# Kernel optimization log

Measured on AMD Instinct MI355X. Metric: run time of the kernel, lower is better.

The kernel has to match this reference:

```python
import jax, jax.numpy as jnp
import numpy as np

WS = 8      # window size
NH = 8      # num heads
DIM = 256   # channels
HD = DIM // NH  # head dim = 32


def _rel_idx():
    ws = WS
    coords = np.stack(np.meshgrid(np.arange(ws), np.arange(ws), indexing='ij'))
    flat = coords.reshape(2, -1)
    rel = (flat[:, :, None] - flat[:, None, :]).transpose(1, 2, 0).copy()
    rel[..., 0] += ws - 1
    rel[..., 1] += ws - 1
    rel[..., 0] *= 2 * ws - 1
    return jnp.asarray(rel.sum(-1))  # [ws*ws, ws*ws]

REL_IDX = _rel_idx()


def _conv(x, w, b=None, pad=0, groups=1):
    out = jax.lax.conv_general_dilated(x, w, (1, 1), [(pad, pad), (pad, pad)],
                                       feature_group_count=groups,
                                       dimension_numbers=('NCHW', 'OIHW', 'NCHW'))
    if b is not None:
        out = out + b[None, :, None, None]
    return out


def _pw(w, x):  # 1x1 conv, no bias
    return jnp.einsum('oc,bchw->bohw', w, x)


def _adaptive_avg_pool(x, s):  # torch AdaptiveAvgPool2d((s,s)) semantics
    B, C, H, W = x.shape
    rows = []
    for i in range(s):
        h0, h1 = (i * H) // s, -((-(i + 1) * H) // s)
        cols = []
        for j in range(s):
            w0, w1 = (j * W) // s, -((-(j + 1) * W) // s)
            cols.append(x[:, :, h0:h1, w0:w1].mean(axis=(2, 3)))
        rows.append(jnp.stack(cols, axis=-1))
    return jnp.stack(rows, axis=-2)  # [B,C,s,s]


def _lowpass(v_img):  # LowPassModule: 4-way channel split, pyramid pool + bilinear up, relu
    B, C, H, W = v_img.shape
    ch = C // 4
    outs = []
    for i, s in enumerate((1, 2, 3, 6)):
        p = _adaptive_avg_pool(v_img[:, i * ch:(i + 1) * ch], s)
        outs.append(jax.image.resize(p, (B, ch, H, W), method='bilinear'))
    return jax.nn.relu(jnp.concatenate(outs, axis=1))


def _avgpool(x, kh, kw, ph, pw):  # AvgPool2d, stride 1, count_include_pad=True
    s = jax.lax.reduce_window(x, 0.0, jax.lax.add, (1, 1, kh, kw), (1, 1, 1, 1),
                              ((0, 0), (0, 0), (ph, ph), (pw, pw)))
    return s / (kh * kw)


def _forward(x, qkv_w, ld1_w, ld2_w, camax_w1, camax_b1, camax_w2, camax_b2,
             caavg_w1, caavg_b1, caavg_w2, caavg_b2, sa_w, sa_b,
             f3_w, f3_b, f5_w, f5_b, f7_w, f7_b, rel_table, dw_w, bn_g, bn_b, pw_w):
    B, C, H, W = x.shape
    ws, h = WS, NH
    d = C // h
    scale = d ** -0.5
    hh, ww = H // ws, W // ws
    # ---- local branch: 1x1 expand -> CBAM -> 1x1 reduce ----
    loc = _pw(ld1_w, x)  # [B,2C,H,W]
    mx = loc.max(axis=(2, 3))
    av = loc.mean(axis=(2, 3))
    wmax = jax.nn.sigmoid(jax.nn.relu(mx @ camax_w1.T + camax_b1) @ camax_w2.T + camax_b2)
    wavg = jax.nn.sigmoid(jax.nn.relu(av @ caavg_w1.T + caavg_b1) @ caavg_w2.T + caavg_b2)
    loc = jax.nn.sigmoid(wmax + wavg)[:, :, None, None] * loc
    cat = jnp.stack([loc.max(axis=1), loc.mean(axis=1)], axis=1)  # [B,2,H,W]
    loc = jax.nn.sigmoid(_conv(cat, sa_w, sa_b, pad=3)) * loc
    loc = _pw(ld2_w, loc)  # [B,C,H,W]
    # ---- windowed qkv (H,W divisible by ws -> reflect pad is a no-op) ----
    qkv = _pw(qkv_w, x)  # [B,3C,H,W]
    t = qkv.reshape(B, 3, h, d, hh, ws, ww, ws)
    t = t.transpose(1, 0, 4, 6, 2, 5, 7, 3).reshape(3, B * hh * ww, h, ws * ws, d)
    q, k = t[0], t[1]
    # df path uses channel decomposition (qkv c h), NOT (qkv h d)
    t2 = qkv.reshape(B, 3, d, h, H * W).transpose(1, 0, 3, 4, 2)  # [3,B,h,N,d]
    df_q, df_v = t2[0], t2[2]
    dots = jnp.einsum('whld,whmd->whlm', q, k) * scale
    bias = rel_table[REL_IDX.reshape(-1)].reshape(ws * ws, ws * ws, h).transpose(2, 0, 1)
    attn = jax.nn.softmax(dots + bias[None], axis=-1)
    # ---- dynamic hi/lo-pass filter ----
    v_img = df_v.transpose(0, 1, 3, 2).reshape(B, h * d, H, W)
    LP = _lowpass(v_img).reshape(B, h, d, H * W).transpose(0, 1, 3, 2)  # [B,h,N,d]
    o1, o2 = 2 * d, 5 * d  # channel splits [64,96,96]
    HP = jnp.concatenate([
        _conv(v_img[:, :o1], f3_w, f3_b, pad=1, groups=o1),
        _conv(v_img[:, o1:o2], f5_w, f5_b, pad=2, groups=3 * d),
        _conv(v_img[:, o2:], f7_w, f7_b, pad=3, groups=3 * d)], axis=1)
    HP = HP.reshape(B, h, d, H * W).transpose(0, 1, 3, 2)
    df = df_q * HP + LP  # [B,h,N,d]
    dfw = df.reshape(B, h, hh, ws, ww, ws, d).transpose(0, 2, 4, 1, 3, 5, 6)
    dfw = dfw.reshape(B * hh * ww, h, ws * ws, d)
    av2 = jnp.einsum('whlm,whmd->whld', attn, dfw)
    img = av2.reshape(B, hh, ww, h, ws, ws, d).transpose(0, 3, 6, 1, 4, 2, 5).reshape(B, C, H, W)
    # ---- directional average pooling + local fuse ----
    px = jnp.pad(img, ((0, 0), (0, 0), (0, 1), (0, 0)), mode='reflect')
    py = jnp.pad(img, ((0, 0), (0, 0), (0, 0), (0, 1)), mode='reflect')
    out = _avgpool(px, ws, 1, ws // 2 - 1, 0) + _avgpool(py, 1, ws, 0, ws // 2 - 1)
    out = out + loc
    out = jnp.pad(out, ((0, 0), (0, 0), (0, 1), (0, 1)), mode='reflect')
    # ---- proj: depthwise k=8 -> BN (eval, running stats 0/1) -> 1x1 ----
    out = _conv(out, dw_w, pad=3, groups=C)
    out = out * (bn_g / jnp.sqrt(1.0 + 1e-5))[None, :, None, None] + bn_b[None, :, None, None]
    out = _pw(pw_w, out)
    return out[:, :, :H, :W]


def setup_inputs() -> dict:
    key = jax.random.key(0)
    ks = jax.random.split(key, 26)
    B, C, H, W = 4, DIM, 128, 128
    d = HD
    f = lambda k, shape, s=0.05: jax.random.normal(k, shape, dtype=jnp.float32) * s
    return {
        'x': jax.random.normal(ks[0], (B, C, H, W), dtype=jnp.float32),
        'qkv_w': f(ks[1], (3 * C, C)),
        'ld1_w': f(ks[2], (2 * C, C)),
        'ld2_w': f(ks[3], (C, 2 * C)),
        'camax_w1': f(ks[4], (C, 2 * C)), 'camax_b1': f(ks[5], (C,)),
        'camax_w2': f(ks[6], (2 * C, C)), 'camax_b2': f(ks[7], (2 * C,)),
        'caavg_w1': f(ks[8], (C, 2 * C)), 'caavg_b1': f(ks[9], (C,)),
        'caavg_w2': f(ks[10], (2 * C, C)), 'caavg_b2': f(ks[11], (2 * C,)),
        'sa_w': f(ks[12], (1, 2, 7, 7)), 'sa_b': f(ks[13], (1,)),
        'f3_w': f(ks[14], (2 * d, 1, 3, 3)), 'f3_b': f(ks[15], (2 * d,)),
        'f5_w': f(ks[16], (3 * d, 1, 5, 5)), 'f5_b': f(ks[17], (3 * d,)),
        'f7_w': f(ks[18], (3 * d, 1, 7, 7)), 'f7_b': f(ks[19], (3 * d,)),
        'rel_table': f(ks[20], ((2 * WS - 1) * (2 * WS - 1), NH), 0.02),
        'dw_w': f(ks[21], (C, 1, WS, WS)),
        'bn_g': 1.0 + f(ks[22], (C,)), 'bn_b': f(ks[23], (C,)),
        'pw_w': f(ks[24], (C, C)),
    }


def reference(x, qkv_w, ld1_w, ld2_w, camax_w1, camax_b1, camax_w2, camax_b2,
              caavg_w1, caavg_b1, caavg_w2, caavg_b2, sa_w, sa_b,
              f3_w, f3_b, f5_w, f5_b, f7_w, f7_b, rel_table, dw_w, bn_g, bn_b, pw_w):
    return _forward(x, qkv_w, ld1_w, ld2_w, camax_w1, camax_b1, camax_w2, camax_b2,
                    caavg_w1, caavg_b1, caavg_w2, caavg_b2, sa_w, sa_b,
                    f3_w, f3_b, f5_w, f5_b, f7_w, f7_b, rel_table, dw_w, bn_g, bn_b, pw_w)
```

## Files before the change

### kernel.cpp

```cpp
#include <hip/hip_runtime.h>
#include <hip/hip_bf16.h>
#include <math.h>

#define B_ 4
#define H_ 128
#define W_ 128
#define N_ 16384

using bf16 = __hip_bfloat16;
typedef short short8 __attribute__((ext_vector_type(8)));
typedef short s16x4 __attribute__((ext_vector_type(4)));
typedef float f32x4 __attribute__((ext_vector_type(4)));

__device__ __forceinline__ float toF(float v) { return v; }
__device__ __forceinline__ float toF(bf16 v) { return __bfloat162float(v); }
__device__ __forceinline__ void storeF(float* p, float v) { *p = v; }
__device__ __forceinline__ void storeF(bf16* p, float v) { *p = __float2bfloat16(v); }

__device__ __forceinline__ unsigned short f2bf(float f) {
  unsigned u = __builtin_bit_cast(unsigned, f);
  unsigned r = (u + 0x7FFFu + ((u >> 16) & 1u)) >> 16;
  return (unsigned short)r;
}
__device__ __forceinline__ short rawbf(float v) { return (short)f2bf(v); }
__device__ __forceinline__ short rawbf(bf16 v) { return __builtin_bit_cast(short, v); }
__device__ __forceinline__ float bfs2f(short s) {
  return __builtin_bit_cast(float, ((unsigned)(unsigned short)s) << 16);
}

__device__ __forceinline__ short8 ld8(const bf16* p) { return *(const short8*)p; }

__device__ __forceinline__ void st8f(float* dst, short8 v) {
  float4 a, b2;
  a.x = bfs2f(v[0]); a.y = bfs2f(v[1]); a.z = bfs2f(v[2]); a.w = bfs2f(v[3]);
  b2.x = bfs2f(v[4]); b2.y = bfs2f(v[5]); b2.z = bfs2f(v[6]); b2.w = bfs2f(v[7]);
  *(float4*)dst = a;
  *(float4*)(dst + 4) = b2;
}

template <typename TX, typename TY>
__global__ __launch_bounds__(256) void gemm_mfma(
    const bf16* __restrict__ Wb, const TX* __restrict__ X, TY* __restrict__ Y, int IC) {
  __shared__ short smA[8192];
  __shared__ short smB[8192];
  int tid = threadIdx.x;
  int lane = tid & 63, w = tid >> 6;
  int wm = w >> 1, wn = w & 1;
  int n0 = blockIdx.x * 128, oc0 = blockIdx.y * 128, b = blockIdx.z;
  const TX* Xb = X + (size_t)b * IC * N_;
  TY* Yb = Y + (size_t)b * (gridDim.y * 128) * N_;
  f32x4 acc[4][4] = {};
  int nB = tid & 127;
  int gB0 = tid >> 7;

  for (int k0 = 0; k0 < IC; k0 += 64) {
    short8 areg[4], breg[4];
#pragma unroll
    for (int i = 0; i < 4; i++) {
      int q = i * 256 + tid;
      int rowA = q >> 3, gA = q & 7;
      areg[i] = ld8(Wb + (size_t)(oc0 + rowA) * IC + k0 + gA * 8);
      int gB = i * 2 + gB0;
      const TX* src = Xb + (size_t)(k0 + gB * 8) * N_ + n0 + nB;
      short8 v;
#pragma unroll
      for (int j = 0; j < 8; j++) v[j] = rawbf(src[(size_t)j * N_]);
      breg[i] = v;
    }
    __syncthreads();
#pragma unroll
    for (int i = 0; i < 4; i++) {
      int q = i * 256 + tid;
      int rowA = q >> 3, gA = q & 7;
      *(short8*)&smA[rowA * 64 + ((gA ^ (rowA & 7)) * 8)] = areg[i];
      int gB = i * 2 + gB0;
      *(short8*)&smB[nB * 64 + ((gB ^ (nB & 7)) * 8)] = breg[i];
    }
    __syncthreads();
#pragma unroll
    for (int ks = 0; ks < 2; ks++) {
      int gk = ks * 4 + (lane >> 4);
      short8 af[4], bfr[4];
#pragma unroll
      for (int mf = 0; mf < 4; mf++) {
        int row = wm * 64 + mf * 16 + (lane & 15);
        af[mf] = *(const short8*)&smA[row * 64 + ((gk ^ (row & 7)) * 8)];
      }
#pragma unroll
      for (int nf = 0; nf < 4; nf++) {
        int nr = wn * 64 + nf * 16 + (lane & 15);
        bfr[nf] = *(const short8*)&smB[nr * 64 + ((gk ^ (nr & 7)) * 8)];
      }
#pragma unroll
      for (int nf = 0; nf < 4; nf++)
#pragma unroll
        for (int mf = 0; mf < 4; mf++)
          acc[mf][nf] = __builtin_amdgcn_mfma_f32_16x16x32_bf16(af[mf], bfr[nf], acc[mf][nf], 0, 0, 0);
    }
    __syncthreads();
  }
#pragma unroll
  for (int mf = 0; mf < 4; mf++)
#pragma unroll
    for (int nf = 0; nf < 4; nf++) {
      int ocr = oc0 + wm * 64 + mf * 16 + ((lane >> 4) << 2);
      int nc = n0 + wn * 64 + nf * 16 + (lane & 15);
#pragma unroll
      for (int j = 0; j < 4; j++)
        storeF(&Yb[(size_t)(ocr + j) * N_ + nc], acc[mf][nf][j]);
    }
}

__global__ __launch_bounds__(256) void gemm_mfmaT(
    const bf16* __restrict__ Wb, const bf16* __restrict__ XT, bf16* __restrict__ Y, int IC) {
  __shared__ short smA[8192];
  __shared__ short smB[8192];
  int tid = threadIdx.x;
  int lane = tid & 63, w = tid >> 6;
  int wm = w >> 1, wn = w & 1;
  int n0 = blockIdx.x * 128, oc0 = blockIdx.y * 128, b = blockIdx.z;
  const bf16* Xb = XT + (size_t)b * N_ * IC;
  bf16* Yb = Y + (size_t)b * (gridDim.y * 128) * N_;
  f32x4 acc[4][4] = {};

  for (int k0 = 0; k0 < IC; k0 += 64) {
    short8 areg[4], breg[4];
#pragma unroll
    for (int i = 0; i < 4; i++) {
      int q = i * 256 + tid;
      int rowA = q >> 3, gA = q & 7;
      areg[i] = ld8(Wb + (size_t)(oc0 + rowA) * IC + k0 + gA * 8);
      breg[i] = ld8(Xb + (size_t)(n0 + rowA) * IC + k0 + gA * 8);
    }
    __syncthreads();
#pragma unroll
    for (int i = 0; i < 4; i++) {
      int q = i * 256 + tid;
      int rowA = q >> 3, gA = q & 7;
      int so = (gA ^ (rowA & 7)) * 8;
      *(short8*)&smA[rowA * 64 + so] = areg[i];
      *(short8*)&smB[rowA * 64 + so] = breg[i];
    }
    __syncthreads();
#pragma unroll
    for (int ks = 0; ks < 2; ks++) {
      int gk = ks * 4 + (lane >> 4);
      short8 af[4], bfr[4];
#pragma unroll
      for (int mf = 0; mf < 4; mf++) {
        int row = wm * 64 + mf * 16 + (lane & 15);
        af[mf] = *(const short8*)&smA[row * 64 + ((gk ^ (row & 7)) * 8)];
      }
#pragma unroll
      for (int nf = 0; nf < 4; nf++) {
        int nr = wn * 64 + nf * 16 + (lane & 15);
        bfr[nf] = *(const short8*)&smB[nr * 64 + ((gk ^ (nr & 7)) * 8)];
      }
#pragma unroll
      for (int nf = 0; nf < 4; nf++)
#pragma unroll
        for (int mf = 0; mf < 4; mf++)
          acc[mf][nf] = __builtin_amdgcn_mfma_f32_16x16x32_bf16(af[mf], bfr[nf], acc[mf][nf], 0, 0, 0);
    }
    __syncthreads();
  }
#pragma unroll
  for (int mf = 0; mf < 4; mf++)
#pragma unroll
    for (int nf = 0; nf < 4; nf++) {
      int ocr = oc0 + wm * 64 + mf * 16 + ((lane >> 4) << 2);
      int nc = n0 + wn * 64 + nf * 16 + (lane & 15);
#pragma unroll
      for (int j = 0; j < 4; j++)
        storeF(&Yb[(size_t)(ocr + j) * N_ + nc], acc[mf][nf][j]);
    }
}

__global__ __launch_bounds__(256) void gemm_qkvT(
    const bf16* __restrict__ Wb, const bf16* __restrict__ XT, bf16* __restrict__ Y, int IC) {
  __shared__ short smA[8192];
  __shared__ short smB[8192];
  int tid = threadIdx.x;
  int lane = tid & 63, w = tid >> 6;
  int wm = w >> 1, wn = w & 1;
  int n0 = blockIdx.x * 128, oc0 = blockIdx.y * 128, b = blockIdx.z;
  const bf16* Xb = XT + (size_t)b * N_ * IC;
  bf16* Yb = Y + (size_t)b * 768 * N_;
  f32x4 acc[4][4] = {};

  for (int k0 = 0; k0 < IC; k0 += 64) {
    short8 areg[4], breg[4];
#pragma unroll
    for (int i = 0; i < 4; i++) {
      int q = i * 256 + tid;
      int rowA = q >> 3, gA = q & 7;
      areg[i] = ld8(Wb + (size_t)(oc0 + rowA) * IC + k0 + gA * 8);
      breg[i] = ld8(Xb + (size_t)(n0 + rowA) * IC + k0 + gA * 8);
    }
    __syncthreads();
#pragma unroll
    for (int i = 0; i < 4; i++) {
      int q = i * 256 + tid;
      int rowA = q >> 3, gA = q & 7;
      int so = (gA ^ (rowA & 7)) * 8;
      *(short8*)&smA[rowA * 64 + so] = areg[i];
      *(short8*)&smB[rowA * 64 + so] = breg[i];
    }
    __syncthreads();
#pragma unroll
    for (int ks = 0; ks < 2; ks++) {
      int gk = ks * 4 + (lane >> 4);
      short8 af[4], bfr[4];
#pragma unroll
      for (int mf = 0; mf < 4; mf++) {
        int row = wm * 64 + mf * 16 + (lane & 15);
        af[mf] = *(const short8*)&smA[row * 64 + ((gk ^ (row & 7)) * 8)];
      }
#pragma unroll
      for (int nf = 0; nf < 4; nf++) {
        int nr = wn * 64 + nf * 16 + (lane & 15);
        bfr[nf] = *(const short8*)&smB[nr * 64 + ((gk ^ (nr & 7)) * 8)];
      }
#pragma unroll
      for (int nf = 0; nf < 4; nf++)
#pragma unroll
        for (int mf = 0; mf < 4; mf++)
          acc[mf][nf] = __builtin_amdgcn_mfma_f32_16x16x32_bf16(af[mf], bfr[nf], acc[mf][nf], 0, 0, 0);
    }
    __syncthreads();
  }
  if (oc0 >= 256 && oc0 < 512) {
    bf16* kT = Yb + (size_t)256 * N_;
#pragma unroll
    for (int mf = 0; mf < 4; mf++)
#pragma unroll
      for (int nf = 0; nf < 4; nf++) {
        int ocr = oc0 + wm * 64 + mf * 16 + ((lane >> 4) << 2);
        int nc = n0 + wn * 64 + nf * 16 + (lane & 15);
        int koff = ocr - 256;
        int head = koff >> 5, dc = koff & 31;
        s16x4 ov;
#pragma unroll
        for (int j = 0; j < 4; j++) ov[j] = rawbf(acc[mf][nf][j]);
        *(s16x4*)&kT[((size_t)head * N_ + nc) * 32 + dc] = ov;
      }
  } else {
#pragma unroll
    for (int mf = 0; mf < 4; mf++)
#pragma unroll
      for (int nf = 0; nf < 4; nf++) {
        int ocr = oc0 + wm * 64 + mf * 16 + ((lane >> 4) << 2);
        int nc = n0 + wn * 64 + nf * 16 + (lane & 15);
#pragma unroll
        for (int j = 0; j < 4; j++)
          storeF(&Yb[(size_t)(ocr + j) * N_ + nc], acc[mf][nf][j]);
      }
  }
}

template <typename TX>
__global__ __launch_bounds__(256) void gemm_qkv(
    const bf16* __restrict__ Wb, const TX* __restrict__ X, bf16* __restrict__ Y, int IC) {
  __shared__ short smA[8192];
  __shared__ short smB[8192];
  int tid = threadIdx.x;
  int lane = tid & 63, w = tid >> 6;
  int wm = w >> 1, wn = w & 1;
  int n0 = blockIdx.x * 128, oc0 = blockIdx.y * 128, b = blockIdx.z;
  const TX* Xb = X + (size_t)b * IC * N_;
  bf16* Yb = Y + (size_t)b * 768 * N_;
  f32x4 acc[4][4] = {};
  int nB = tid & 127;
  int gB0 = tid >> 7;

  for (int k0 = 0; k0 < IC; k0 += 64) {
    short8 areg[4], breg[4];
#pragma unroll
    for (int i = 0; i < 4; i++) {
      int q = i * 256 + tid;
      int rowA = q >> 3, gA = q & 7;
      areg[i] = ld8(Wb + (size_t)(oc0 + rowA) * IC + k0 + gA * 8);
      int gB = i * 2 + gB0;
      const TX* src = Xb + (size_t)(k0 + gB * 8) * N_ + n0 + nB;
      short8 v;
#pragma unroll
      for (int j = 0; j < 8; j++) v[j] = rawbf(src[(size_t)j * N_]);
      breg[i] = v;
    }
    __syncthreads();
#pragma unroll
    for (int i = 0; i < 4; i++) {
      int q = i * 256 + tid;
      int rowA = q >> 3, gA = q & 7;
      *(short8*)&smA[rowA * 64 + ((gA ^ (rowA & 7)) * 8)] = areg[i];
      int gB = i * 2 + gB0;
      *(short8*)&smB[nB * 64 + ((gB ^ (nB & 7)) * 8)] = breg[i];
    }
    __syncthreads();
#pragma unroll
    for (int ks = 0; ks < 2; ks++) {
      int gk = ks * 4 + (lane >> 4);
      short8 af[4], bfr[4];
#pragma unroll
      for (int mf = 0; mf < 4; mf++) {
        int row = wm * 64 + mf * 16 + (lane & 15);
        af[mf] = *(const short8*)&smA[row * 64 + ((gk ^ (row & 7)) * 8)];
      }
#pragma unroll
      for (int nf = 0; nf < 4; nf++) {
        int nr = wn * 64 + nf * 16 + (lane & 15);
        bfr[nf] = *(const short8*)&smB[nr * 64 + ((gk ^ (nr & 7)) * 8)];
      }
#pragma unroll
      for (int nf = 0; nf < 4; nf++)
#pragma unroll
        for (int mf = 0; mf < 4; mf++)
          acc[mf][nf] = __builtin_amdgcn_mfma_f32_16x16x32_bf16(af[mf], bfr[nf], acc[mf][nf], 0, 0, 0);
    }
    __syncthreads();
  }
  if (oc0 >= 256 && oc0 < 512) {
    bf16* kT = Yb + (size_t)256 * N_;
#pragma unroll
    for (int mf = 0; mf < 4; mf++)
#pragma unroll
      for (int nf = 0; nf < 4; nf++) {
        int ocr = oc0 + wm * 64 + mf * 16 + ((lane >> 4) << 2);
        int nc = n0 + wn * 64 + nf * 16 + (lane & 15);
        int koff = ocr - 256;
        int head = koff >> 5, dc = koff & 31;
        s16x4 ov;
#pragma unroll
        for (int j = 0; j < 4; j++) ov[j] = rawbf(acc[mf][nf][j]);
        *(s16x4*)&kT[((size_t)head * N_ + nc) * 32 + dc] = ov;
      }
  } else {
#pragma unroll
    for (int mf = 0; mf < 4; mf++)
#pragma unroll
      for (int nf = 0; nf < 4; nf++) {
        int ocr = oc0 + wm * 64 + mf * 16 + ((lane >> 4) << 2);
        int nc = n0 + wn * 64 + nf * 16 + (lane & 15);
#pragma unroll
        for (int j = 0; j < 4; j++)
          storeF(&Yb[(size_t)(ocr + j) * N_ + nc], acc[mf][nf][j]);
      }
  }
}

__global__ __launch_bounds__(256) void gemm_mfma_sc(
    const bf16* __restrict__ Wb, const bf16* __restrict__ X, bf16* __restrict__ Y, int IC,
    const float* __restrict__ svec, const float* __restrict__ samap) {
  __shared__ short smA[8192];
  __shared__ short smB[8192];
  int tid = threadIdx.x;
  int lane = tid & 63, w = tid >> 6;
  int wm = w >> 1, wn = w & 1;
  int n0 = blockIdx.x * 128, oc0 = blockIdx.y * 128, b = blockIdx.z;
  const bf16* Xb = X + (size_t)b * IC * N_;
  bf16* Yb = Y + (size_t)b * (gridDim.y * 128) * N_;
  f32x4 acc[4][4] = {};
  int nB = tid & 127;
  int gB0 = tid >> 7;
  const float* sv = svec + b * 512;
  float sm = samap[b * N_ + n0 + nB];

  for (int k0 = 0; k0 < IC; k0 += 64) {
    short8 areg[4], breg[4];
#pragma unroll
    for (int i = 0; i < 4; i++) {
      int q = i * 256 + tid;
      int rowA = q >> 3, gA = q & 7;
      areg[i] = ld8(Wb + (size_t)(oc0 + rowA) * IC + k0 + gA * 8);
      int gB = i * 2 + gB0;
      int c0 = k0 + gB * 8;
      const bf16* src = Xb + (size_t)c0 * N_ + n0 + nB;
      short8 v;
#pragma unroll
      for (int j = 0; j < 8; j++)
        v[j] = rawbf(bfs2f(rawbf(src[(size_t)j * N_])) * sv[c0 + j] * sm);
      breg[i] = v;
    }
    __syncthreads();
#pragma unroll
    for (int i = 0; i < 4; i++) {
      int q = i * 256 + tid;
      int rowA = q >> 3, gA = q & 7;
      *(short8*)&smA[rowA * 64 + ((gA ^ (rowA & 7)) * 8)] = areg[i];
      int gB = i * 2 + gB0;
      *(short8*)&smB[nB * 64 + ((gB ^ (nB & 7)) * 8)] = breg[i];
    }
    __syncthreads();
#pragma unroll
    for (int ks = 0; ks < 2; ks++) {
      int gk = ks * 4 + (lane >> 4);
      short8 af[4], bfr[4];
#pragma unroll
      for (int mf = 0; mf < 4; mf++) {
        int row = wm * 64 + mf * 16 + (lane & 15);
        af[mf] = *(const short8*)&smA[row * 64 + ((gk ^ (row & 7)) * 8)];
      }
#pragma unroll
      for (int nf = 0; nf < 4; nf++) {
        int nr = wn * 64 + nf * 16 + (lane & 15);
        bfr[nf] = *(const short8*)&smB[nr * 64 + ((gk ^ (nr & 7)) * 8)];
      }
#pragma unroll
      for (int nf = 0; nf < 4; nf++)
#pragma unroll
        for (int mf = 0; mf < 4; mf++)
          acc[mf][nf] = __builtin_amdgcn_mfma_f32_16x16x32_bf16(af[mf], bfr[nf], acc[mf][nf], 0, 0, 0);
    }
    __syncthreads();
  }
#pragma unroll
  for (int mf = 0; mf < 4; mf++)
#pragma unroll
    for (int nf = 0; nf < 4; nf++) {
      int ocr = oc0 + wm * 64 + mf * 16 + ((lane >> 4) << 2);
      int nc = n0 + wn * 64 + nf * 16 + (lane & 15);
#pragma unroll
      for (int j = 0; j < 4; j++)
        storeF(&Yb[(size_t)(ocr + j) * N_ + nc], acc[mf][nf][j]);
    }
}

__global__ __launch_bounds__(256) void k_cvt(const float* __restrict__ s,
                                             bf16* __restrict__ d, int n) {
  int i = blockIdx.x * 256 + threadIdx.x;
  if (i < n) d[i] = __float2bfloat16(s[i]);
}

__global__ __launch_bounds__(256) void k_cvtT(const float* __restrict__ x,
                                              bf16* __restrict__ xT) {
  int ct = blockIdx.x, nt = blockIdx.y, b = blockIdx.z;
  int c0 = ct * 64, n0 = nt * 128;
  __shared__ float t[64][129];
  int tid = threadIdx.x;
  const float* xb_ = x + ((size_t)b * 256 + c0) * N_ + n0;
#pragma unroll
  for (int i = 0; i < 8; i++) {
    int q = i * 256 + tid;
    int r = q >> 5, col4 = q & 31;
    float4 v = *(const float4*)&xb_[(size_t)r * N_ + col4 * 4];
    t[r][col4 * 4 + 0] = v.x; t[r][col4 * 4 + 1] = v.y;
    t[r][col4 * 4 + 2] = v.z; t[r][col4 * 4 + 3] = v.w;
  }
  __syncthreads();
  bf16* dst = xT + ((size_t)b * N_ + n0) * 256 + c0;
#pragma unroll
  for (int i = 0; i < 4; i++) {
    int q = i * 256 + tid;
    int nl = q >> 3, oct = q & 7;
    short8 v;
#pragma unroll
    for (int j = 0; j < 8; j++) v[j] = rawbf(t[oct * 8 + j][nl]);
    *(short8*)&dst[(size_t)nl * 256 + oct * 8] = v;
  }
}

template <int S>
__device__ __forceinline__ void lp_body(const bf16* __restrict__ src,
                                        float* __restrict__ poolout,
                                        float (*part)[6], int tid) {
  int row = tid >> 1, xh = (tid & 1) << 6;
  float partial[6] = {0.f, 0.f, 0.f, 0.f, 0.f, 0.f};
  const bf16* rp = src + row * W_ + xh;
#pragma unroll
  for (int o = 0; o < 8; o++) {
    short8 v = ld8(rp + o * 8);
#pragma unroll
    for (int e = 0; e < 8; e++) {
      float f = bfs2f(v[e]);
      int x = xh + o * 8 + e;
#pragma unroll
      for (int j = 0; j < S; j++) {
        int w0 = (j * W_) / S;
        int w1 = ((j + 1) * W_ + S - 1) / S;
        if (x >= w0 && x < w1) partial[j] += f;
      }
    }
  }
#pragma unroll
  for (int j = 0; j < S; j++) part[tid][j] = partial[j];
  __syncthreads();
  if (tid < S * S) {
    int i = tid / S, j = tid % S;
    int h0 = (i * H_) / S, h1 = ((i + 1) * H_ + S - 1) / S;
    int w0 = (j * W_) / S, w1 = ((j + 1) * W_ + S - 1) / S;
    float sum = 0.f;
    for (int r2 = h0; r2 < h1; r2++) sum += part[r2 * 2][j] + part[r2 * 2 + 1][j];
    poolout[tid] = sum / (float)((h1 - h0) * (w1 - w0));
  }
}

__global__ __launch_bounds__(256) void k_lp_pool(const bf16* __restrict__ qkv,
                                                 float* __restrict__ pools) {
  int cc = blockIdx.x, b = blockIdx.y;
  __shared__ float part[256][6];
  int vch = 512 + (cc & 31) * 8 + (cc >> 5);
  const bf16* src = qkv + ((size_t)b * 768 + vch) * N_;
  float* po = pools + ((size_t)b * 256 + cc) * 36;
  int tid = threadIdx.x;
  int g = cc >> 6;
  if (g == 0)      lp_body<1>(src, po, part, tid);
  else if (g == 1) lp_body<2>(src, po, part, tid);
  else if (g == 2) lp_body<3>(src, po, part, tid);
  else             lp_body<6>(src, po, part, tid);
}

template <int KSZ>
__device__ __forceinline__ void hp_conv4(const float (*patch)[136], const float* wsm,
                                         int rs4, int cg4, float acc[4][4]) {
  constexpr int ROFF = 3 - KSZ / 2;
  constexpr int COFF = 4 - KSZ / 2;
#pragma unroll
  for (int pr = ROFF; pr < ROFF + KSZ + 3; pr++) {
    float val[12];
    const float* row = &patch[rs4 + pr][cg4];
    *(float4*)&val[0] = *(const float4*)&row[0];
    *(float4*)&val[4] = *(const float4*)&row[4];
    *(float4*)&val[8] = *(const float4*)&row[8];
#pragma unroll
    for (int j = 0; j < 4; j++) {
      int u = pr - ROFF - j;
      if (u >= 0 && u < KSZ) {
#pragma unroll
        for (int v = 0; v < KSZ; v++) {
          float wv = wsm[u * KSZ + v];
#pragma unroll
          for (int c = 0; c < 4; c++) acc[j][c] += val[c + v + COFF] * wv;
        }
      }
    }
  }
}

__global__ __launch_bounds__(256) void k_dffuse(const bf16* __restrict__ qkv,
    const float* __restrict__ pools,
    const float* __restrict__ f3w, const float* __restrict__ f3b,
    const float* __restrict__ f5w, const float* __restrict__ f5b,
    const float* __restrict__ f7w, const float* __restrict__ f7b,
    bf16* __restrict__ df) {
  int b = blockIdx.z, cc = blockIdx.y, ty0 = blockIdx.x * 32;
  __shared__ float patch[38][136];
  __shared__ float wsm[49];
  int tid = threadIdx.x;
  int vch = 512 + (cc & 31) * 8 + (cc >> 5);
  const bf16* src = qkv + ((size_t)b * 768 + vch) * N_;
  int ksz; const float* wp; float bias;
  if (cc < 64)       { ksz = 3; wp = f3w + cc * 9;          bias = f3b[cc]; }
  else if (cc < 160) { ksz = 5; wp = f5w + (cc - 64) * 25;  bias = f5b[cc - 64]; }
  else               { ksz = 7; wp = f7w + (cc - 160) * 49; bias = f7b[cc - 160]; }
  if (tid < ksz * ksz) wsm[tid] = wp[tid];
  float4 z4 = make_float4(0.f, 0.f, 0.f, 0.f);
  for (int i4 = tid; i4 < 1292; i4 += 256) ((float4*)patch)[i4] = z4;
  __syncthreads();
  for (int slot = tid; slot < 38 * 16; slot += 256) {
    int py = slot >> 4, seg = slot & 15;
    int gy = ty0 - 3 + py;
    if (gy >= 0 && gy < H_)
      st8f(&patch[py][4 + seg * 8], ld8(&src[gy * W_ + seg * 8]));
  }
  __syncthreads();
  int rs4 = (tid >> 5) * 4, cg4 = (tid & 31) * 4;
  float acc[4][4] = {{bias, bias, bias, bias}, {bias, bias, bias, bias},
                     {bias, bias, bias, bias}, {bias, bias, bias, bias}};
  if (cc < 64)       hp_conv4<3>(patch, wsm, rs4, cg4, acc);
  else if (cc < 160) hp_conv4<5>(patch, wsm, rs4, cg4, acc);
  else               hp_conv4<7>(patch, wsm, rs4, cg4, acc);
  const int S[4] = {1, 2, 3, 6};
  int s = S[cc >> 6];
  const float* pl = pools + ((size_t)b * 256 + cc) * 36;
  int qch = (cc & 31) * 8 + (cc >> 5);
  const bf16* qsrc = qkv + ((size_t)b * 768 + qch) * N_;
#pragma unroll
  for (int j = 0; j < 4; j++) {
    int y = ty0 + rs4 + j;
    float fy = (y + 0.5f) * s * (1.0f / 128.f) - 0.5f;
    int i0r = (int)floorf(fy); float tyf = fy - i0r;
    int i1 = min(max(i0r + 1, 0), s - 1);
    int i0 = min(max(i0r, 0), s - 1);
    s16x4 qv = *(const s16x4*)&qsrc[y * W_ + cg4];
    s16x4 ov;
#pragma unroll
    for (int c = 0; c < 4; c++) {
      int x = cg4 + c;
      float fx = (x + 0.5f) * s * (1.0f / 128.f) - 0.5f;
      int j0r = (int)floorf(fx); float txf = fx - j0r;
      int j1 = min(max(j0r + 1, 0), s - 1);
      int j0 = min(max(j0r, 0), s - 1);
      float v00 = pl[i0 * s + j0], v01 = pl[i0 * s + j1];
      float v10 = pl[i1 * s + j0], v11 = pl[i1 * s + j1];
      float lp = (1.f - tyf) * ((1.f - txf) * v00 + txf * v01) +
                 tyf * ((1.f - txf) * v10 + txf * v11);
      lp = fmaxf(lp, 0.f);
      ov[c] = rawbf(bfs2f(qv[c]) * acc[j][c] + lp);
    }
    *(s16x4*)&df[((size_t)b * 256 + cc) * N_ + y * W_ + cg4] = ov;
  }
}

__global__ __launch_bounds__(256) void k_attn(const bf16* __restrict__ qkv,
    bf16* __restrict__ df, const float* __restrict__ rel) {
  int b = blockIdx.z, head = blockIdx.y, wg = blockIdx.x;
  int wh = wg >> 2, wc4 = wg & 3;
  __shared__ short P[4][4096];
  __shared__ float biasLds[4][228];
  int tid = threadIdx.x, lane = tid & 63, w = tid >> 6;
  int wc = wc4 * 4 + w;
  short* Pw = P[w];
  float* bw = biasLds[w];
  int lr = lane & 15, lo = lane >> 4;
  int nwin = (wh * 8) * W_ + wc * 8;
  for (int i = lane; i < 225; i += 64) bw[i] = rel[i * 8 + head];
  const bf16* qb = qkv + ((size_t)b * 768 + head * 32 + lo * 8) * N_;
  const bf16* kT = qkv + ((size_t)b * 768 + 256) * N_ + (size_t)head * N_ * 32;
  short8 af[4], bf4[4];
#pragma unroll
  for (int mf = 0; mf < 4; mf++) {
    int l = mf * 16 + lr;
    int n = nwin + (l >> 3) * W_ + (l & 7);
#pragma unroll
    for (int j = 0; j < 8; j++) af[mf][j] = rawbf(qb[(size_t)j * N_ + n]);
    bf4[mf] = ld8(&kT[(size_t)n * 32 + lo * 8]);
  }
  const bf16* dbase = df + ((size_t)b * 256 + head * 32) * N_;
  short8 db[2][2];
#pragma unroll
  for (int ks = 0; ks < 2; ks++)
#pragma unroll
    for (int nf = 0; nf < 2; nf++) {
      int dc = nf * 16 + lr;
      int r = ks * 4 + lo;
      db[ks][nf] = ld8(dbase + (size_t)dc * N_ + nwin + r * W_);
    }
  f32x4 acc[4][4] = {};
#pragma unroll
  for (int nf = 0; nf < 4; nf++)
#pragma unroll
    for (int mf = 0; mf < 4; mf++)
      acc[mf][nf] = __builtin_amdgcn_mfma_f32_16x16x32_bf16(af[mf], bf4[nf], acc[mf][nf], 0, 0, 0);
  const float scale = 0.17677669529663687f;
#pragma unroll
  for (int mf = 0; mf < 4; mf++)
#pragma unroll
    for (int j = 0; j < 4; j++) {
      int lrow = mf * 16 + lo * 4 + j;
      int r1 = lrow >> 3, c1 = lrow & 7;
#pragma unroll
      for (int nf = 0; nf < 4; nf++) {
        int m = nf * 16 + lr;
        acc[mf][nf][j] = acc[mf][nf][j] * scale +
                         bw[(r1 - (m >> 3) + 7) * 15 + (c1 - (m & 7) + 7)];
      }
      float mx = fmaxf(fmaxf(acc[mf][0][j], acc[mf][1][j]),
                       fmaxf(acc[mf][2][j], acc[mf][3][j]));
      mx = fmaxf(mx, __shfl_xor(mx, 1));
      mx = fmaxf(mx, __shfl_xor(mx, 2));
      mx = fmaxf(mx, __shfl_xor(mx, 4));
      mx = fmaxf(mx, __shfl_xor(mx, 8));
      float s = 0.f;
#pragma unroll
      for (int nf = 0; nf < 4; nf++) {
        acc[mf][nf][j] = __expf(acc[mf][nf][j] - mx);
        s += acc[mf][nf][j];
      }
      s += __shfl_xor(s, 1); s += __shfl_xor(s, 2);
      s += __shfl_xor(s, 4); s += __shfl_xor(s, 8);
      float inv = 1.0f / s;
#pragma unroll
      for (int nf = 0; nf < 4; nf++) {
        int m = nf * 16 + lr;
        Pw[lrow * 64 + (((m >> 3) ^ (lrow & 7)) * 8) + (m & 7)] = rawbf(acc[mf][nf][j] * inv);
      }
    }
  __syncthreads();
  f32x4 acc2[4][2] = {};
#pragma unroll
  for (int ks = 0; ks < 2; ks++) {
    short8 pa[4];
#pragma unroll
    for (int mf = 0; mf < 4; mf++) {
      int row = mf * 16 + lr;
      pa[mf] = *(const short8*)&Pw[row * 64 + (((ks * 4 + lo) ^ (row & 7)) * 8)];
    }
#pragma unroll
    for (int nf = 0; nf < 2; nf++)
#pragma unroll
      for (int mf = 0; mf < 4; mf++)
        acc2[mf][nf] = __builtin_amdgcn_mfma_f32_16x16x32_bf16(pa[mf], db[ks][nf], acc2[mf][nf], 0, 0, 0);
  }
#pragma unroll
  for (int mf = 0; mf < 4; mf++)
#pragma unroll
    for (int nf = 0; nf < 2; nf++) {
      int ll = mf * 16 + lo * 4;
      int dc = nf * 16 + lr;
      s16x4 ov;
#pragma unroll
      for (int j = 0; j < 4; j++) ov[j] = rawbf(acc2[mf][nf][j]);
      int n = nwin + (ll >> 3) * W_ + (ll & 7);
      *(s16x4*)&df[((size_t)b * 256 + head * 32 + dc) * N_ + n] = ov;
    }
}

__global__ __launch_bounds__(256) void k_chstats(const bf16* __restrict__ loc,
    float* __restrict__ mx, float* __restrict__ av) {
  int c = blockIdx.x, b = blockIdx.y;
  const bf16* p = loc + ((size_t)b * 512 + c) * N_;
  int tid = threadIdx.x;
  float m = -1e30f, s = 0.f;
  for (int i = tid * 8; i < N_; i += 2048) {
    short8 v = *(const short8*)&p[i];
#pragma unroll
    for (int j = 0; j < 8; j++) { float f = bfs2f(v[j]); m = fmaxf(m, f); s += f; }
  }
  __shared__ float rm[256], rs[256];
  rm[tid] = m; rs[tid] = s;
  __syncthreads();
  for (int off = 128; off > 0; off >>= 1) {
    if (tid < off) {
      rm[tid] = fmaxf(rm[tid], rm[tid + off]);
      rs[tid] += rs[tid + off];
    }
    __syncthreads();
  }
  if (tid == 0) { mx[b * 512 + c] = rm[0]; av[b * 512 + c] = rs[0] / (float)N_; }
}

__global__ __launch_bounds__(256) void k_mlp1(const float* __restrict__ mx,
    const float* __restrict__ av,
    const float* __restrict__ w1m, const float* __restrict__ b1m,
    const float* __restrict__ w1a, const float* __restrict__ b1a,
    float* __restrict__ hidden) {
  int path = blockIdx.z, b = blockIdx.y, j0 = blockIdx.x * 64;
  const float* stats = (path ? av : mx) + b * 512;
  const float* w1 = path ? w1a : w1m;
  const float* b1 = path ? b1a : b1m;
  int tid = threadIdx.x, lane = tid & 63, wv = tid >> 6;
#pragma unroll
  for (int jj = 0; jj < 16; jj++) {
    int j = j0 + wv * 16 + jj;
    float a = 0.f;
#pragma unroll
    for (int t = 0; t < 8; t++) {
      int i = lane + t * 64;
      a += stats[i] * w1[j * 512 + i];
    }
#pragma unroll
    for (int off = 32; off > 0; off >>= 1) a += __shfl_xor(a, off);
    if (lane == 0) hidden[(path * 4 + b) * 256 + j] = fmaxf(a + b1[j], 0.f);
  }
}

__global__ __launch_bounds__(256) void k_mlp2(const float* __restrict__ hidden,
    const float* __restrict__ w2m, const float* __restrict__ b2m,
    const float* __restrict__ w2a, const float* __restrict__ b2a,
    float* __restrict__ svec) {
  int b = blockIdx.y, o0 = blockIdx.x * 64;
  const float* hm = hidden + b * 256;
  const float* ha = hidden + (4 + b) * 256;
  int tid = threadIdx.x, lane = tid & 63, wv = tid >> 6;
#pragma unroll
  for (int oo = 0; oo < 16; oo++) {
    int o = o0 + wv * 16 + oo;
    float sm = 0.f, sa = 0.f;
#pragma unroll
    for (int t = 0; t < 4; t++) {
      int jj = lane + t * 64;
      sm += hm[jj] * w2m[o * 256 + jj];
      sa += ha[jj] * w2a[o * 256 + jj];
    }
#pragma unroll
    for (int off = 32; off > 0; off >>= 1) {
      sm += __shfl_xor(sm, off);
      sa += __shfl_xor(sa, off);
    }
    if (lane == 0) {
      float wm = 1.f / (1.f + __expf(-(sm + b2m[o])));
      float wa = 1.f / (1.f + __expf(-(sa + b2a[o])));
      svec[b * 512 + o] = 1.f / (1.f + __expf(-(wm + wa)));
    }
  }
}

__global__ __launch_bounds__(256) void k_cat(const bf16* __restrict__ loc,
    const float* __restrict__ svec, float* __restrict__ catmax, float* __restrict__ catmean) {
  int b = blockIdx.y;
  int n2 = (blockIdx.x * 256 + threadIdx.x) * 2;
  const bf16* lb = loc + (size_t)b * 512 * N_;
  const float* sv = svec + b * 512;
  float m0 = -1e30f, m1 = -1e30f, s0 = 0.f, s1 = 0.f;
#pragma unroll 4
  for (int c = 0; c < 512; c++) {
    unsigned u = *(const unsigned*)&lb[(size_t)c * N_ + n2];
    float sc = sv[c];
    float f0 = __builtin_bit_cast(float, u << 16) * sc;
    float f1 = __builtin_bit_cast(float, u & 0xffff0000u) * sc;
    m0 = fmaxf(m0, f0); s0 += f0;
    m1 = fmaxf(m1, f1); s1 += f1;
  }
  catmax[b * N_ + n2] = m0;     catmax[b * N_ + n2 + 1] = m1;
  catmean[b * N_ + n2] = s0 * (1.f / 512.f);
  catmean[b * N_ + n2 + 1] = s1 * (1.f / 512.f);
}

__global__ __launch_bounds__(256) void k_sa(const float* __restrict__ catmax,
    const float* __restrict__ catmean, const float* __restrict__ saw,
    const float* __restrict__ sab, float* __restrict__ samap) {
  int b = blockIdx.y;
  int n = blockIdx.x * 256 + threadIdx.x;
  int y = n >> 7, x = n & 127;
  float acc = sab[0];
  for (int u = 0; u < 7; u++) {
    int yy = y + u - 3;
    if (yy < 0 || yy >= H_) continue;
    for (int v = 0; v < 7; v++) {
      int xx = x + v - 3;
      if (xx < 0 || xx >= W_) continue;
      int nn = b * N_ + yy * W_ + xx;
      acc += catmax[nn] * saw[u * 7 + v] + catmean[nn] * saw[49 + u * 7 + v];
    }
  }
  samap[b * N_ + n] = 1.f / (1.f + __expf(-acc));
}

__global__ __launch_bounds__(256) void k_out1(const bf16* __restrict__ img,
    const bf16* __restrict__ locout, bf16* __restrict__ out1) {
  int b = blockIdx.z, c = blockIdx.y, ty0 = blockIdx.x * 32;
  __shared__ float patch[39][136];
  int tid = threadIdx.x;
  const bf16* p = img + ((size_t)b * 256 + c) * N_;
  float4 z4 = make_float4(0.f, 0.f, 0.f, 0.f);
  for (int i4 = tid; i4 < 1326; i4 += 256) ((float4*)patch)[i4] = z4;
  __syncthreads();
  for (int slot = tid; slot < 39 * 16; slot += 256) {
    int py = slot >> 4, seg = slot & 15;
    int gy = ty0 - 3 + py;
    if (gy >= 0 && gy <= 128) {
      int yy = (gy == 128) ? 126 : gy;
      st8f(&patch[py][4 + seg * 8], ld8(&p[yy * W_ + seg * 8]));
    }
  }
  if (tid < 39) {
    int gy = ty0 - 3 + tid;
    if (gy >= 0 && gy <= 128) {
      int yy = (gy == 128) ? 126 : gy;
      patch[tid][132] = toF(p[yy * W_ + 126]);
    }
  }
  __syncthreads();
  int rs4 = (tid >> 5) * 4, cg4 = (tid & 31) * 4;
  float accv[4][4] = {};
  float acch[4][4] = {};
#pragma unroll
  for (int pr = 0; pr < 11; pr++) {
    float val[12];
    const float* row = &patch[rs4 + pr][cg4];
    *(float4*)&val[0] = *(const float4*)&row[0];
    *(float4*)&val[4] = *(const float4*)&row[4];
    *(float4*)&val[8] = *(const float4*)&row[8];
#pragma unroll
    for (int j = 0; j < 4; j++) {
      int u = pr - j;
      if (u >= 0 && u < 8) {
#pragma unroll
        for (int cc2 = 0; cc2 < 4; cc2++) accv[j][cc2] += val[cc2 + 4];
        if (u == 3) {
#pragma unroll
          for (int off = 1; off <= 8; off++)
#pragma unroll
            for (int cc2 = 0; cc2 < 4; cc2++) acch[j][cc2] += val[cc2 + off];
        }
      }
    }
  }
#pragma unroll
  for (int j = 0; j < 4; j++) {
    int y = ty0 + rs4 + j;
    size_t o = ((size_t)b * 256 + c) * N_ + y * W_ + cg4;
    s16x4 lo = *(const s16x4*)&locout[o];
    s16x4 ov;
#pragma unroll
    for (int cc2 = 0; cc2 < 4; cc2++)
      ov[cc2] = rawbf(0.125f * (accv[j][cc2] + acch[j][cc2]) + bfs2f(lo[cc2]));
    *(s16x4*)&out1[o] = ov;
  }
}

__global__ __launch_bounds__(256) void k_dw(const bf16* __restrict__ out1,
    const float* __restrict__ dww, const float* __restrict__ bng,
    const float* __restrict__ bnb, bf16* __restrict__ dwo) {
  int b = blockIdx.z, c = blockIdx.y, ty0 = blockIdx.x * 32;
  __shared__ float patch[39][136];
  __shared__ float wsm[64];
  int tid = threadIdx.x;
  const bf16* p = out1 + ((size_t)b * 256 + c) * N_;
  if (tid < 64) wsm[tid] = dww[c * 64 + tid];
  float4 z4 = make_float4(0.f, 0.f, 0.f, 0.f);
  for (int i4 = tid; i4 < 1326; i4 += 256) ((float4*)patch)[i4] = z4;
  __syncthreads();
  for (int slot = tid; slot < 39 * 16; slot += 256) {
    int py = slot >> 4, seg = slot & 15;
    int gy = ty0 - 3 + py;
    if (gy >= 0 && gy <= 128) {
      int yy = (gy == 128) ? 126 : gy;
      st8f(&patch[py][4 + seg * 8], ld8(&p[yy * W_ + seg * 8]));
    }
  }
  if (tid < 39) {
    int gy = ty0 - 3 + tid;
    if (gy >= 0 && gy <= 128) {
      int yy = (gy == 128) ? 126 : gy;
      patch[tid][132] = toF(p[yy * W_ + 126]);
    }
  }
  __syncthreads();
  int rs4 = (tid >> 5) * 4, cg4 = (tid & 31) * 4;
  float acc[4][4] = {};
#pragma unroll
  for (int pr = 0; pr < 11; pr++) {
    float val[12];
    const float* row = &patch[rs4 + pr][cg4];
    *(float4*)&val[0] = *(const float4*)&row[0];
    *(float4*)&val[4] = *(const float4*)&row[4];
    *(float4*)&val[8] = *(const float4*)&row[8];
#pragma unroll
    for (int j = 0; j < 4; j++) {
      int u = pr - j;
      if (u >= 0 && u < 8) {
#pragma unroll
        for (int v = 0; v < 8; v++) {
          float wv = wsm[u * 8 + v];
#pragma unroll
          for (int cc2 = 0; cc2 < 4; cc2++) acc[j][cc2] += val[cc2 + v + 1] * wv;
        }
      }
    }
  }
  float g = bng[c] * rsqrtf(1.0f + 1e-5f);
  float bb = bnb[c];
#pragma unroll
  for (int j = 0; j < 4; j++) {
    int y = ty0 + rs4 + j;
    s16x4 ov;
#pragma unroll
    for (int cc2 = 0; cc2 < 4; cc2++) ov[cc2] = rawbf(acc[j][cc2] * g + bb);
    *(s16x4*)&dwo[((size_t)b * 256 + c) * N_ + y * W_ + cg4] = ov;
  }
}

extern "C" void kernel_launch(void* const* d_in, const int* in_sizes, int n_in,
                              void* d_out, int out_size, void* d_ws, size_t ws_size,
                              hipStream_t stream) {
  const float* x        = (const float*)d_in[0];
  const float* qkv_w    = (const float*)d_in[1];
  const float* ld1_w    = (const float*)d_in[2];
  const float* ld2_w    = (const float*)d_in[3];
  const float* camax_w1 = (const float*)d_in[4];
  const float* camax_b1 = (const float*)d_in[5];
  const float* camax_w2 = (const float*)d_in[6];
  const float* camax_b2 = (const float*)d_in[7];
  const float* caavg_w1 = (const float*)d_in[8];
  const float* caavg_b1 = (const float*)d_in[9];
  const float* caavg_w2 = (const float*)d_in[10];
  const float* caavg_b2 = (const float*)d_in[11];
  const float* sa_w     = (const float*)d_in[12];
  const float* sa_b     = (const float*)d_in[13];
  const float* f3_w     = (const float*)d_in[14];
  const float* f3_b     = (const float*)d_in[15];
  const float* f5_w     = (const float*)d_in[16];
  const float* f5_b     = (const float*)d_in[17];
  const float* f7_w     = (const float*)d_in[18];
  const float* f7_b     = (const float*)d_in[19];
  const float* rel_tab  = (const float*)d_in[20];
  const float* dw_w     = (const float*)d_in[21];
  const float* bn_g     = (const float*)d_in[22];
  const float* bn_b     = (const float*)d_in[23];
  const float* pw_w     = (const float*)d_in[24];
  float* out = (float*)d_out;

  char* wsb = (char*)d_ws;
  bf16* qkvb   = (bf16*)(wsb);
  bf16* dfb    = (bf16*)(wsb + 100663296);
  bf16* locb   = (bf16*)(wsb);
  bf16* locout = (bf16*)(wsb + 67108864);
  bf16* out1   = (bf16*)(wsb);
  bf16* dwo    = (bf16*)(wsb + 33554432);
  float* small = (float*)(wsb + 134217728);
  float* pools   = small;
  float* mx      = small + 36864;
  float* av      = small + 38912;
  float* svec    = small + 40960;
  float* catmax  = small + 43008;
  float* catmean = small + 108544;
  float* samap   = small + 174080;
  float* hidden  = catmax;
  bf16* wq  = (bf16*)(wsb + 135176192);
  bf16* wl1 = wq  + 196608;
  bf16* wl2 = wl1 + 131072;
  bf16* wpw = wl2 + 131072;
  bf16* xT = (bf16*)(wsb + 136224768);
  bool use_xb = ws_size >= (size_t)170000000;

  dim3 blk(256);
  k_cvt<<<dim3(768), blk, 0, stream>>>(qkv_w, wq, 196608);
  k_cvt<<<dim3(512), blk, 0, stream>>>(ld1_w, wl1, 131072);
  k_cvt<<<dim3(512), blk, 0, stream>>>(ld2_w, wl2, 131072);
  k_cvt<<<dim3(256), blk, 0, stream>>>(pw_w, wpw, 65536);
  if (use_xb) k_cvtT<<<dim3(4, 128, 4), blk, 0, stream>>>(x, xT);

  if (use_xb) gemm_qkvT<<<dim3(128, 6, 4), blk, 0, stream>>>(wq, xT, qkvb, 256);
  else        gemm_qkv<float><<<dim3(128, 6, 4), blk, 0, stream>>>(wq, x, qkvb, 256);
  k_lp_pool<<<dim3(256, 4), blk, 0, stream>>>(qkvb, pools);
  k_dffuse<<<dim3(4, 256, 4), blk, 0, stream>>>(qkvb, pools, f3_w, f3_b, f5_w, f5_b,
                                                f7_w, f7_b, dfb);
  k_attn<<<dim3(64, 8, 4), blk, 0, stream>>>(qkvb, dfb, rel_tab);
  if (use_xb) gemm_mfmaT<<<dim3(128, 4, 4), blk, 0, stream>>>(wl1, xT, locb, 256);
  else        gemm_mfma<float, bf16><<<dim3(128, 4, 4), blk, 0, stream>>>(wl1, x, locb, 256);
  k_chstats<<<dim3(512, 4), blk, 0, stream>>>(locb, mx, av);
  k_mlp1<<<dim3(4, 4, 2), blk, 0, stream>>>(mx, av, camax_w1, camax_b1,
                                            caavg_w1, caavg_b1, hidden);
  k_mlp2<<<dim3(8, 4), blk, 0, stream>>>(hidden, camax_w2, camax_b2,
                                         caavg_w2, caavg_b2, svec);
  k_cat<<<dim3(32, 4), blk, 0, stream>>>(locb, svec, catmax, catmean);
  k_sa<<<dim3(64, 4), blk, 0, stream>>>(catmax, catmean, sa_w, sa_b, samap);
  gemm_mfma_sc<<<dim3(128, 2, 4), blk, 0, stream>>>(wl2, locb, locout, 512, svec, samap);
  k_out1<<<dim3(4, 256, 4), blk, 0, stream>>>(dfb, locout, out1);
  k_dw<<<dim3(4, 256, 4), blk, 0, stream>>>(out1, dw_w, bn_g, bn_b, dwo);
  gemm_mfma<bf16, float><<<dim3(128, 2, 4), blk, 0, stream>>>(wpw, dwo, out, 256);
}
```

Baseline: 425.4 us.

## Fuse out1 stencil and depthwise conv into one kernel via shared-memory halo

Merges the out1 kernel (window-sum stencil plus local output) and the depthwise 8x8 conv with BN into a single kernel. The combined kernel loads a larger halo patch, computes the out1 tile including its halo into shared memory with bf16 rounding, then runs the depthwise conv from LDS. This drops one launch and a full bf16 write and read of the out1 tensor through global memory. In exchange it recomputes the halo rows and uses more shared memory per block, which can lower occupancy.

New measurement: 438.0 us. +3.0%, slower.

```diff
diff --git a/kernel.cpp b/kernel.cpp
--- a/kernel.cpp
+++ b/kernel.cpp
@@ -826,103 +826,78 @@
   samap[b * N_ + n] = 1.f / (1.f + __expf(-acc));
 }
 
-__global__ __launch_bounds__(256) void k_out1(const bf16* __restrict__ img,
-    const bf16* __restrict__ locout, bf16* __restrict__ out1) {
+__global__ __launch_bounds__(256) void k_odw(const bf16* __restrict__ img,
+    const bf16* __restrict__ locout,
+    const float* __restrict__ dww, const float* __restrict__ bng,
+    const float* __restrict__ bnb, bf16* __restrict__ dwo) {
   int b = blockIdx.z, c = blockIdx.y, ty0 = blockIdx.x * 32;
-  __shared__ float patch[39][136];
+  __shared__ float patch[46][136];
+  __shared__ float o1buf[39][136];
+  __shared__ float wsm[64];
   int tid = threadIdx.x;
   const bf16* p = img + ((size_t)b * 256 + c) * N_;
+  const bf16* lb = locout + ((size_t)b * 256 + c) * N_;
+  if (tid < 64) wsm[tid] = dww[c * 64 + tid];
   float4 z4 = make_float4(0.f, 0.f, 0.f, 0.f);
-  for (int i4 = tid; i4 < 1326; i4 += 256) ((float4*)patch)[i4] = z4;
+  for (int i4 = tid; i4 < 1564; i4 += 256) ((float4*)patch)[i4] = z4;
+  for (int i4 = tid; i4 < 1326; i4 += 256) ((float4*)o1buf)[i4] = z4;
   __syncthreads();
-  for (int slot = tid; slot < 39 * 16; slot += 256) {
+  for (int slot = tid; slot < 46 * 16; slot += 256) {
     int py = slot >> 4, seg = slot & 15;
-    int gy = ty0 - 3 + py;
+    int gy = ty0 - 6 + py;
     if (gy >= 0 && gy <= 128) {
       int yy = (gy == 128) ? 126 : gy;
       st8f(&patch[py][4 + seg * 8], ld8(&p[yy * W_ + seg * 8]));
     }
   }
-  if (tid < 39) {
-    int gy = ty0 - 3 + tid;
+  if (tid < 46) {
+    int gy = ty0 - 6 + tid;
     if (gy >= 0 && gy <= 128) {
       int yy = (gy == 128) ? 126 : gy;
       patch[tid][132] = toF(p[yy * W_ + 126]);
     }
   }
   __syncthreads();
-  int rs4 = (tid >> 5) * 4, cg4 = (tid & 31) * 4;
-  float accv[4][4] = {};
-  float acch[4][4] = {};
-#pragma unroll
-  for (int pr = 0; pr < 11; pr++) {
-    float val[12];
-    const float* row = &patch[rs4 + pr][cg4];
-    *(float4*)&val[0] = *(const float4*)&row[0];
-    *(float4*)&val[4] = *(const float4*)&row[4];
-    *(float4*)&val[8] = *(const float4*)&row[8];
-#pragma unroll
-    for (int j = 0; j < 4; j++) {
-      int u = pr - j;
-      if (u >= 0 && u < 8) {
-#pragma unroll
-        for (int cc2 = 0; cc2 < 4; cc2++) accv[j][cc2] += val[cc2 + 4];
-        if (u == 3) {
-#pragma unroll
-          for (int off = 1; off <= 8; off++)
-#pragma unroll
-            for (int cc2 = 0; cc2 < 4; cc2++) acch[j][cc2] += val[cc2 + off];
-        }
-      }
-    }
-  }
-#pragma unroll
-  for (int j = 0; j < 4; j++) {
-    int y = ty0 + rs4 + j;
-    size_t o = ((size_t)b * 256 + c) * N_ + y * W_ + cg4;
-    s16x4 lo = *(const s16x4*)&locout[o];
-    s16x4 ov;
-#pragma unroll
-    for (int cc2 = 0; cc2 < 4; cc2++)
-      ov[cc2] = rawbf(0.125f * (accv[j][cc2] + acch[j][cc2]) + bfs2f(lo[cc2]));
-    *(s16x4*)&out1[o] = ov;
-  }
-}
-
-__global__ __launch_bounds__(256) void k_dw(const bf16* __restrict__ out1,
-    const float* __restrict__ dww, const float* __restrict__ bng,
-    const float* __restrict__ bnb, bf16* __restrict__ dwo) {
-  int b = blockIdx.z, c = blockIdx.y, ty0 = blockIdx.x * 32;
-  __shared__ float patch[39][136];
-  __shared__ float wsm[64];
-  int tid = threadIdx.x;
-  const bf16* p = out1 + ((size_t)b * 256 + c) * N_;
-  if (tid < 64) wsm[tid] = dww[c * 64 + tid];
-  float4 z4 = make_float4(0.f, 0.f, 0.f, 0.f);
-  for (int i4 = tid; i4 < 1326; i4 += 256) ((float4*)patch)[i4] = z4;
+  for (int slot = tid; slot < 624; slot += 256) {
+    int q = slot >> 4, oct = slot & 15;
+    int oy = ty0 - 3 + q;
+    int eff = (oy == 128) ? 126 : oy;
+    if (eff >= 0 && eff <= 127) {
+      float val[16];
+      const float* hrow = &patch[q + 3][oct * 8];
+      *(float4*)&val[0]  = *(const float4*)&hrow[0];
+      *(float4*)&val[4]  = *(const float4*)&hrow[4];
+      *(float4*)&val[8]  = *(const float4*)&hrow[8];
+      *(float4*)&val[12] = *(const float4*)&hrow[12];
+      float sv[8] = {};
+#pragma unroll
+      for (int u = 0; u < 8; u++) {
+        const float* vrow = &patch[q + u][oct * 8 + 4];
+        float4 a = *(const float4*)&vrow[0];
+        float4 bb2 = *(const float4*)&vrow[4];
+        sv[0] += a.x; sv[1] += a.y; sv[2] += a.z; sv[3] += a.w;
+        sv[4] += bb2.x; sv[5] += bb2.y; sv[6] += bb2.z; sv[7] += bb2.w;
+      }
+      short8 lo8 = ld8(&lb[eff * W_ + oct * 8]);
+#pragma unroll
+      for (int e = 0; e < 8; e++) {
+        float sh = 0.f;
+#pragma unroll
+        for (int off = 1; off <= 8; off++) sh += val[e + off];
+        float v = 0.125f * (sv[e] + sh) + bfs2f(lo8[e]);
+        o1buf[q][4 + oct * 8 + e] = bfs2f(rawbf(v));
+      }
+    }
+  }
   __syncthreads();
-  for (int slot = tid; slot < 39 * 16; slot += 256) {
-    int py = slot >> 4, seg = slot & 15;
-    int gy = ty0 - 3 + py;
-    if (gy >= 0 && gy <= 128) {
-      int yy = (gy == 128) ? 126 : gy;
-      st8f(&patch[py][4 + seg * 8], ld8(&p[yy * W_ + seg * 8]));
-    }
-  }
-  if (tid < 39) {
-    int gy = ty0 - 3 + tid;
-    if (gy >= 0 && gy <= 128) {
-      int yy = (gy == 128) ? 126 : gy;
-      patch[tid][132] = toF(p[yy * W_ + 126]);
-    }
-  }
+  if (tid < 39) o1buf[tid][132] = o1buf[tid][130];
   __syncthreads();
   int rs4 = (tid >> 5) * 4, cg4 = (tid & 31) * 4;
   float acc[4][4] = {};
 #pragma unroll
   for (int pr = 0; pr < 11; pr++) {
     float val[12];
-    const float* row = &patch[rs4 + pr][cg4];
+    const float* row = &o1buf[rs4 + pr][cg4];
     *(float4*)&val[0] = *(const float4*)&row[0];
     *(float4*)&val[4] = *(const float4*)&row[4];
     *(float4*)&val[8] = *(const float4*)&row[8];
@@ -986,7 +961,6 @@
   bf16* dfb    = (bf16*)(wsb + 100663296);
   bf16* locb   = (bf16*)(wsb);
   bf16* locout = (bf16*)(wsb + 67108864);
-  bf16* out1   = (bf16*)(wsb);
   bf16* dwo    = (bf16*)(wsb + 33554432);
   float* small = (float*)(wsb + 134217728);
   float* pools   = small;
@@ -1027,7 +1001,6 @@
   k_cat<<<dim3(32, 4), blk, 0, stream>>>(locb, svec, catmax, catmean);
   k_sa<<<dim3(64, 4), blk, 0, stream>>>(catmax, catmean, sa_w, sa_b, samap);
   gemm_mfma_sc<<<dim3(128, 2, 4), blk, 0, stream>>>(wl2, locb, locout, 512, svec, samap);
-  k_out1<<<dim3(4, 256, 4), blk, 0, stream>>>(dfb, locout, out1);
-  k_dw<<<dim3(4, 256, 4), blk, 0, stream>>>(out1, dw_w, bn_g, bn_b, dwo);
+  k_odw<<<dim3(4, 256, 4), blk, 0, stream>>>(dfb, locout, dw_w, bn_g, bn_b, dwo);
   gemm_mfma<bf16, float><<<dim3(128, 2, 4), blk, 0, stream>>>(wpw, dwo, out, 256);
 }
```
